# Kernel tuning notes

Hardware: AMD Instinct MI355X
Metric: run time of the kernel (lower is better)

The kernel has to match this reference:

```python
import jax, jax.numpy as jnp
import numpy as np

N_NODES = 50000
N_EDGES = 600000
F_IN = 128
HID = 128
N_GRAPHS = 512
N_CLASSES = 2


def _sage_conv(x, src, dst, Wl, Wr, b, n_nodes):
    # PyG SAGEConv (aggr='mean'): out = lin_l(mean_{j in N(i)} x_j) + lin_r(x_i)
    msg_sum = jax.ops.segment_sum(x[src], dst, num_segments=n_nodes)  # [N, F]
    deg = jax.ops.segment_sum(jnp.ones((src.shape[0],), x.dtype), dst, num_segments=n_nodes)
    agg = msg_sum / jnp.maximum(deg, 1.0)[:, None]
    return agg @ Wl + b + x @ Wr


def setup_inputs() -> dict:
    key = jax.random.key(0)
    ks = jax.random.split(key, 16)
    x = jax.random.normal(ks[0], (N_NODES, F_IN), dtype=jnp.float32)
    edge_index = jax.random.randint(ks[1], (2, N_EDGES), 0, N_NODES, dtype=jnp.int64)
    batch = jnp.sort(jax.random.randint(ks[2], (N_NODES,), 0, N_GRAPHS, dtype=jnp.int64))
    inp = {"x": x, "edge_index": edge_index, "batch": batch, "num_graphs": N_GRAPHS}
    # SAGEConv params (glorot-ish scale)
    dims = [(F_IN, HID), (HID, HID), (HID, HID), (HID, HID)]
    for i, (din, dout) in enumerate(dims, start=1):
        s = 1.0 / np.sqrt(din)
        inp[f"Wl{i}"] = jax.random.normal(ks[2 + 3 * i], (din, dout), dtype=jnp.float32) * s
        inp[f"Wr{i}"] = jax.random.normal(ks[3 + 3 * i], (din, dout), dtype=jnp.float32) * s
        inp[f"b{i}"] = jnp.zeros((dout,), dtype=jnp.float32)
    inp["Wf1"] = jax.random.normal(ks[3], (HID, 128), dtype=jnp.float32) / np.sqrt(HID)
    inp["bf1"] = jnp.zeros((128,), dtype=jnp.float32)
    inp["Wf2"] = jax.random.normal(ks[4], (128, N_CLASSES), dtype=jnp.float32) / np.sqrt(128.0)
    inp["bf2"] = jnp.zeros((N_CLASSES,), dtype=jnp.float32)
    return inp


def reference(x, edge_index, batch, num_graphs,
              Wl1, Wr1, b1, Wl2, Wr2, b2, Wl3, Wr3, b3, Wl4, Wr4, b4,
              Wf1, bf1, Wf2, bf2):
    src, dst = edge_index[0], edge_index[1]
    n = x.shape[0]
    h = jax.nn.relu(_sage_conv(x, src, dst, Wl1, Wr1, b1, n))
    h = jax.nn.relu(_sage_conv(h, src, dst, Wl2, Wr2, b2, n))
    h = jax.nn.relu(_sage_conv(h, src, dst, Wl3, Wr3, b3, n))
    h = jax.nn.relu(_sage_conv(h, src, dst, Wl4, Wr4, b4, n))
    # global_mean_pool over graphs
    pooled_sum = jax.ops.segment_sum(h, batch, num_segments=num_graphs)
    counts = jax.ops.segment_sum(jnp.ones((n,), h.dtype), batch, num_segments=num_graphs)
    pooled = pooled_sum / jnp.maximum(counts, 1.0)[:, None]
    emb = pooled @ Wf1 + bf1
    # dropout p=0.5 is identity in eval mode
    out = emb @ Wf2 + bf2
    return out
```

## Files before the change

### kernel.cpp

```cpp
#include <hip/hip_runtime.h>

#define N_NODES   50000
#define N_EDGES   600000
#define F         128
#define N_GRAPHS  512
#define MROWS     32
#define ASTRIDE   264
#define ALSTRIDE  136
#define NB_SCAN   196
#define EB        8

typedef short          short8   __attribute__((ext_vector_type(8)));
typedef float          f32x4    __attribute__((ext_vector_type(4)));
typedef unsigned int   uint4_t  __attribute__((ext_vector_type(4)));

__device__ __forceinline__ void split_bf16(float v, short& hi, short& lo) {
    unsigned u  = __float_as_uint(v);
    unsigned hb = u & 0xFFFF0000u;
    hi = (short)(u >> 16);
    float rem = v - __uint_as_float(hb);
    lo = (short)(__float_as_uint(rem) >> 16);
}

__device__ __forceinline__ unsigned short f2bf_rne(float f) {
    unsigned u = __float_as_uint(f);
    u += 0x7FFFu + ((u >> 16) & 1u);
    return (unsigned short)(u >> 16);
}

__global__ __launch_bounds__(256) void prepA_kernel(
    const float* __restrict__ x, unsigned short* __restrict__ xb,
    unsigned short* __restrict__ hb0, unsigned short* __restrict__ hb1,
    const float* __restrict__ Wl0, const float* __restrict__ Wr0,
    const float* __restrict__ Wl1, const float* __restrict__ Wr1,
    const float* __restrict__ Wl2, const float* __restrict__ Wr2,
    const float* __restrict__ Wl3, const float* __restrict__ Wr3,
    short* __restrict__ wtbase,
    const int* __restrict__ dst, int* __restrict__ deg)
{
    const int gid  = blockIdx.x * 256 + threadIdx.x;
    const int nthr = gridDim.x * 256;

    if (gid < 48) {
        int bsel = gid >> 4, c = gid & 15;
        unsigned short* p = (bsel == 0 ? xb : bsel == 1 ? hb0 : hb1)
                            + (size_t)N_NODES * F + c * 8;
        short8 z = {0,0,0,0,0,0,0,0};
        *(short8*)p = z;
    }

    for (int i = gid; i < (N_NODES * F) / 8; i += nthr) {
        float4 a = ((const float4*)x)[2 * i];
        float4 b = ((const float4*)x)[2 * i + 1];
        short8 o;
        o[0] = (short)f2bf_rne(a.x); o[1] = (short)f2bf_rne(a.y);
        o[2] = (short)f2bf_rne(a.z); o[3] = (short)f2bf_rne(a.w);
        o[4] = (short)f2bf_rne(b.x); o[5] = (short)f2bf_rne(b.y);
        o[6] = (short)f2bf_rne(b.z); o[7] = (short)f2bf_rne(b.w);
        ((short8*)xb)[i] = o;
    }

    for (int gt = gid; gt < 131072; gt += nthr) {
        int l = gt >> 15;
        int t = gt & 32767;
        const float* Wl; const float* Wr;
        switch (l) {
            case 0:  Wl = Wl0; Wr = Wr0; break;
            case 1:  Wl = Wl1; Wr = Wr1; break;
            case 2:  Wl = Wl2; Wr = Wr2; break;
            default: Wl = Wl3; Wr = Wr3; break;
        }
        int n = t >> 8, k = t & 255;
        float w = (k < F) ? Wl[k * F + n] : Wr[(k - F) * F + n];
        short h, lo;
        split_bf16(w, h, lo);
        short* hi_plane = wtbase + (size_t)l * 65536;
        hi_plane[t]         = h;
        hi_plane[32768 + t] = lo;
    }

    for (int e = gid; e < N_EDGES; e += nthr) atomicAdd(&deg[dst[e]], 1);
}

__global__ __launch_bounds__(256) void bsum_kernel(const int* __restrict__ deg,
                                                   int* __restrict__ bsum) {
    int i = blockIdx.x * 256 + threadIdx.x;
    int v = (i < N_NODES) ? deg[i] : 0;
    #pragma unroll
    for (int off = 32; off > 0; off >>= 1) v += __shfl_down(v, off, 64);
    __shared__ int wsum[4];
    if ((threadIdx.x & 63) == 0) wsum[threadIdx.x >> 6] = v;
    __syncthreads();
    if (threadIdx.x == 0) bsum[blockIdx.x] = wsum[0] + wsum[1] + wsum[2] + wsum[3];
}

__global__ __launch_bounds__(256) void scan_apply_kernel(
    const int* __restrict__ deg, const int* __restrict__ bsum,
    int* __restrict__ row_start, int* __restrict__ cursor,
    float* __restrict__ inv_deg)
{
    __shared__ int s[256];
    const int b = blockIdx.x, t = threadIdx.x;

    int v = (t < NB_SCAN) ? bsum[t] : 0;
    s[t] = v;
    __syncthreads();
    for (int off = 1; off < 256; off <<= 1) {
        int xv  = s[t];
        int add = (t >= off) ? s[t - off] : 0;
        __syncthreads();
        s[t] = xv + add;
        __syncthreads();
    }
    const int boff = (b == 0) ? 0 : s[b - 1];
    __syncthreads();

    int i = b * 256 + t;
    int d = (i < N_NODES) ? deg[i] : 0;
    s[t] = d;
    __syncthreads();
    for (int off = 1; off < 256; off <<= 1) {
        int xv  = s[t];
        int add = (t >= off) ? s[t - off] : 0;
        __syncthreads();
        s[t] = xv + add;
        __syncthreads();
    }
    int excl = s[t] - d + boff;
    if (i < N_NODES) {
        row_start[i] = excl;
        cursor[i]    = excl;
        inv_deg[i]   = 1.0f / fmaxf((float)d, 1.0f);
    }
    if (b == 0 && t == 0) row_start[N_NODES] = N_EDGES;
}

__global__ void fill_kernel(const int* __restrict__ src, const int* __restrict__ dst,
                            int* __restrict__ cursor, int* __restrict__ eidx) {
    int e = blockIdx.x * blockDim.x + threadIdx.x;
    if (e < N_EDGES) {
        int p = atomicAdd(&cursor[dst[e]], 1);
        eidx[p] = src[e];
    }
}

__global__ __launch_bounds__(512) void layer_kernel(
    const unsigned short* __restrict__ hb_in, const int* __restrict__ row_start,
    const int* __restrict__ eidx, const float* __restrict__ inv_deg,
    const short* __restrict__ wt_hi, const short* __restrict__ wt_lo,
    const float* __restrict__ b, unsigned short* __restrict__ hb_out)
{
    __shared__ short Ahi[MROWS][ASTRIDE];
    __shared__ short Alo[MROWS][ALSTRIDE];

    const int t    = threadIdx.x;
    const int base = blockIdx.x * MROWS;

    {
        const int c8  = t & 15;
        const int rr  = t >> 4;
        const int row = base + rr;
        const bool v  = (row < N_NODES);

        int a0 = 0, na = 0;
        float sc = 0.0f;
        if (v) {
            a0 = row_start[row];
            na = row_start[row + 1] - a0;
            sc = inv_deg[row];
        }

        short8 selfv = {0,0,0,0,0,0,0,0};
        if (v) selfv = *(const short8*)(hb_in + (size_t)row * F + c8 * 8);

        float acc[8] = {0,0,0,0,0,0,0,0};
        for (int eo = 0; eo < na; eo += EB) {
            int idx[EB];
            #pragma unroll
            for (int u = 0; u < EB; ++u) {
                bool ok = (eo + u) < na;
                int  sl = ok ? a0 + eo + u : a0;
                int  ia = eidx[sl];
                idx[u] = ok ? ia : N_NODES;
            }
            #pragma unroll
            for (int u = 0; u < EB; ++u) {
                short8 hv = *(const short8*)(hb_in + (size_t)idx[u] * F + c8 * 8);
                uint4_t uw = *(const uint4_t*)&hv;
                #pragma unroll
                for (int q = 0; q < 4; ++q) {
                    unsigned wq = uw[q];
                    acc[2 * q]     += __uint_as_float(wq << 16);
                    acc[2 * q + 1] += __uint_as_float(wq & 0xFFFF0000u);
                }
            }
        }

        short8 h8, l8;
        #pragma unroll
        for (int k = 0; k < 8; ++k) {
            short h, l;
            split_bf16(acc[k] * sc, h, l);
            h8[k] = h; l8[k] = l;
        }
        *(short8*)&Ahi[rr][c8 * 8] = h8;
        *(short8*)&Alo[rr][c8 * 8] = l8;
        *(short8*)&Ahi[rr][F + c8 * 8] = selfv;
    }
    __syncthreads();

    const int w    = t >> 6;
    const int lane = t & 63;
    const int m    = lane & 15;
    const int quad = lane >> 4;
    const int n0   = w * 16 + m;

    f32x4 acc0 = {0,0,0,0};
    f32x4 acc1 = {0,0,0,0};

    #pragma unroll
    for (int ks = 0; ks < 4; ++ks) {
        const int ko = ks * 32 + quad * 8;
        short8 ah0 = *(const short8*)&Ahi[m][ko];
        short8 ah1 = *(const short8*)&Ahi[16 + m][ko];
        short8 al0 = *(const short8*)&Alo[m][ko];
        short8 al1 = *(const short8*)&Alo[16 + m][ko];
        short8 bh  = *(const short8*)&wt_hi[(size_t)n0 * 256 + ko];
        short8 bl  = *(const short8*)&wt_lo[(size_t)n0 * 256 + ko];

        acc0 = __builtin_amdgcn_mfma_f32_16x16x32_bf16(ah0, bh, acc0, 0, 0, 0);
        acc0 = __builtin_amdgcn_mfma_f32_16x16x32_bf16(ah0, bl, acc0, 0, 0, 0);
        acc0 = __builtin_amdgcn_mfma_f32_16x16x32_bf16(al0, bh, acc0, 0, 0, 0);

        acc1 = __builtin_amdgcn_mfma_f32_16x16x32_bf16(ah1, bh, acc1, 0, 0, 0);
        acc1 = __builtin_amdgcn_mfma_f32_16x16x32_bf16(ah1, bl, acc1, 0, 0, 0);
        acc1 = __builtin_amdgcn_mfma_f32_16x16x32_bf16(al1, bh, acc1, 0, 0, 0);
    }
    #pragma unroll
    for (int ks = 4; ks < 8; ++ks) {
        const int ko = ks * 32 + quad * 8;
        short8 ah0 = *(const short8*)&Ahi[m][ko];
        short8 ah1 = *(const short8*)&Ahi[16 + m][ko];
        short8 bh  = *(const short8*)&wt_hi[(size_t)n0 * 256 + ko];
        short8 bl  = *(const short8*)&wt_lo[(size_t)n0 * 256 + ko];

        acc0 = __builtin_amdgcn_mfma_f32_16x16x32_bf16(ah0, bh, acc0, 0, 0, 0);
        acc0 = __builtin_amdgcn_mfma_f32_16x16x32_bf16(ah0, bl, acc0, 0, 0, 0);

        acc1 = __builtin_amdgcn_mfma_f32_16x16x32_bf16(ah1, bh, acc1, 0, 0, 0);
        acc1 = __builtin_amdgcn_mfma_f32_16x16x32_bf16(ah1, bl, acc1, 0, 0, 0);
    }

    float bj = b[n0];
    #pragma unroll
    for (int reg = 0; reg < 4; ++reg) {
        int r0 = base + quad * 4 + reg;
        int r1 = r0 + 16;
        if (r0 < N_NODES)
            hb_out[(size_t)r0 * F + n0] = f2bf_rne(fmaxf(acc0[reg] + bj, 0.0f));
        if (r1 < N_NODES)
            hb_out[(size_t)r1 * F + n0] = f2bf_rne(fmaxf(acc1[reg] + bj, 0.0f));
    }
}

__global__ __launch_bounds__(512) void poolhead_kernel(
    const int* __restrict__ batch, const unsigned short* __restrict__ hb,
    const float* __restrict__ Wf1, const float* __restrict__ bf1,
    const float* __restrict__ Wf2, const float* __restrict__ bf2,
    float* __restrict__ out)
{
    const int g   = blockIdx.x;
    const int j   = threadIdx.x & 127;
    const int grp = threadIdx.x >> 7;

    int lo = 0, hi = N_NODES;
    while (lo < hi) { int m = (lo + hi) >> 1; if (batch[m] < g) lo = m + 1; else hi = m; }
    int start = lo;
    hi = N_NODES;
    while (lo < hi) { int m = (lo + hi) >> 1; if (batch[m] <= g) lo = m + 1; else hi = m; }
    int end = lo;

    float acc = 0.0f;
    for (int r = start + grp; r < end; r += 4)
        acc += __uint_as_float((unsigned)hb[(size_t)r * F + j] << 16);

    __shared__ float part[4][F];
    __shared__ float p[F];
    __shared__ float emb[F];
    part[grp][j] = acc;
    __syncthreads();
    if (grp == 0) {
        float tot = (part[0][j] + part[1][j]) + (part[2][j] + part[3][j]);
        p[j] = tot / fmaxf((float)(end - start), 1.0f);
    }
    __syncthreads();

    float e = 0.0f;
    #pragma unroll 8
    for (int k = grp * 32; k < grp * 32 + 32; ++k) e += p[k] * Wf1[k * F + j];
    part[grp][j] = e;
    __syncthreads();
    if (grp == 0)
        emb[j] = (part[0][j] + part[1][j]) + (part[2][j] + part[3][j]) + bf1[j];
    __syncthreads();

    if (threadIdx.x < 2) {
        float o = bf2[threadIdx.x];
        for (int k = 0; k < F; ++k) o += emb[k] * Wf2[k * 2 + threadIdx.x];
        out[(size_t)g * 2 + threadIdx.x] = o;
    }
}

extern "C" void kernel_launch(void* const* d_in, const int* in_sizes, int n_in,
                              void* d_out, int out_size, void* d_ws, size_t ws_size,
                              hipStream_t stream) {
    const float* x     = (const float*)d_in[0];
    const int*   ei    = (const int*)d_in[1];
    const int*   src   = ei;
    const int*   dst   = ei + N_EDGES;
    const int*   batch = (const int*)d_in[2];
    const float* Wl0 = (const float*)d_in[4];
    const float* Wr0 = (const float*)d_in[5];
    const float* Wl1 = (const float*)d_in[7];
    const float* Wr1 = (const float*)d_in[8];
    const float* Wl2 = (const float*)d_in[10];
    const float* Wr2 = (const float*)d_in[11];
    const float* Wl3 = (const float*)d_in[13];
    const float* Wr3 = (const float*)d_in[14];
    const float* bb[4] = {(const float*)d_in[6],  (const float*)d_in[9],
                          (const float*)d_in[12], (const float*)d_in[15]};
    const float* Wf1 = (const float*)d_in[16];
    const float* bf1 = (const float*)d_in[17];
    const float* Wf2 = (const float*)d_in[18];
    const float* bf2 = (const float*)d_in[19];
    float* out = (float*)d_out;

    const size_t HSZ = (size_t)(N_NODES + 1) * F;
    unsigned short* XB  = (unsigned short*)d_ws;
    unsigned short* HB0 = XB + HSZ;
    unsigned short* HB1 = HB0 + HSZ;
    float* inv_deg   = (float*)(HB1 + HSZ);
    int*   row_start = (int*)(inv_deg + N_NODES);
    int*   cursor    = row_start + N_NODES + 1;
    int*   eidx      = cursor + N_NODES;
    int*   deg_i     = eidx + N_EDGES;
    int*   bsum      = deg_i + N_NODES;
    short* wtbase    = (short*)(bsum + 256);

    (void)hipMemsetAsync(deg_i, 0, N_NODES * sizeof(int), stream);

    prepA_kernel<<<1024, 256, 0, stream>>>(
        x, XB, HB0, HB1, Wl0, Wr0, Wl1, Wr1, Wl2, Wr2, Wl3, Wr3,
        wtbase, dst, deg_i);
    bsum_kernel<<<NB_SCAN, 256, 0, stream>>>(deg_i, bsum);
    scan_apply_kernel<<<NB_SCAN, 256, 0, stream>>>(deg_i, bsum, row_start, cursor, inv_deg);
    fill_kernel<<<(N_EDGES + 255) / 256, 256, 0, stream>>>(src, dst, cursor, eidx);

    const int layer_blocks = (N_NODES + MROWS - 1) / MROWS;
    const unsigned short* hin = XB;
    unsigned short* buf[2] = {HB0, HB1};
    for (int l = 0; l < 4; ++l) {
        unsigned short* tgt = buf[l & 1];
        const short* whi = wtbase + (size_t)l * 65536;
        const short* wlo = whi + 32768;
        layer_kernel<<<layer_blocks, 512, 0, stream>>>(
            hin, row_start, eidx, inv_deg, whi, wlo, bb[l], tgt);
        hin = tgt;
    }

    poolhead_kernel<<<N_GRAPHS, 512, 0, stream>>>(batch, hin, Wf1, bf1, Wf2, bf2, out);
}
```

Baseline: 401.4 us.

## Record edge slot during degree count and merge scan kernels

The degree-counting atomic now also returns each edge's position within its destination bucket and stores it. The CSR fill can then write directly to row_start+pos without a second atomic pass or a cursor array. The two-kernel block-sum plus scan is merged into one kernel in which each block redundantly sums all earlier counts to get its offset. This removes one launch and one round of contended atomics, at the cost of an extra 600k-int pos array and quadratic redundant reads in the scan.

Result: no change. 406.2 us, median of 2 (+1.2%).

```diff
diff --git a/kernel.cpp b/kernel.cpp
--- a/kernel.cpp
+++ b/kernel.cpp
@@ -36,7 +36,7 @@
     const float* __restrict__ Wl2, const float* __restrict__ Wr2,
     const float* __restrict__ Wl3, const float* __restrict__ Wr3,
     short* __restrict__ wtbase,
-    const int* __restrict__ dst, int* __restrict__ deg)
+    const int* __restrict__ dst, int* __restrict__ cnt, int* __restrict__ pos)
 {
     const int gid  = blockIdx.x * 256 + threadIdx.x;
     const int nthr = gridDim.x * 256;
@@ -79,31 +79,30 @@
         hi_plane[32768 + t] = lo;
     }
 
-    for (int e = gid; e < N_EDGES; e += nthr) atomicAdd(&deg[dst[e]], 1);
-}
-
-__global__ __launch_bounds__(256) void bsum_kernel(const int* __restrict__ deg,
-                                                   int* __restrict__ bsum) {
-    int i = blockIdx.x * 256 + threadIdx.x;
-    int v = (i < N_NODES) ? deg[i] : 0;
-    #pragma unroll
-    for (int off = 32; off > 0; off >>= 1) v += __shfl_down(v, off, 64);
-    __shared__ int wsum[4];
-    if ((threadIdx.x & 63) == 0) wsum[threadIdx.x >> 6] = v;
-    __syncthreads();
-    if (threadIdx.x == 0) bsum[blockIdx.x] = wsum[0] + wsum[1] + wsum[2] + wsum[3];
-}
-
-__global__ __launch_bounds__(256) void scan_apply_kernel(
-    const int* __restrict__ deg, const int* __restrict__ bsum,
-    int* __restrict__ row_start, int* __restrict__ cursor,
-    float* __restrict__ inv_deg)
+    for (int e = gid; e < N_EDGES; e += nthr)
+        pos[e] = atomicAdd(&cnt[dst[e]], 1);
+}
+
+__global__ __launch_bounds__(256) void scan2_kernel(
+    const int* __restrict__ cnt,
+    int* __restrict__ row_start, float* __restrict__ inv_deg)
 {
     __shared__ int s[256];
+    __shared__ int red[4];
     const int b = blockIdx.x, t = threadIdx.x;
 
-    int v = (t < NB_SCAN) ? bsum[t] : 0;
-    s[t] = v;
+    int partial = 0;
+    const int lim = b * 256;
+    for (int i = t; i < lim; i += 256) partial += cnt[i];
+    #pragma unroll
+    for (int off = 32; off > 0; off >>= 1) partial += __shfl_down(partial, off, 64);
+    if ((t & 63) == 0) red[t >> 6] = partial;
+    __syncthreads();
+    const int boff = red[0] + red[1] + red[2] + red[3];
+
+    int i = lim + t;
+    int d = (i < N_NODES) ? cnt[i] : 0;
+    s[t] = d;
     __syncthreads();
     for (int off = 1; off < 256; off <<= 1) {
         int xv  = s[t];
@@ -112,36 +111,20 @@
         s[t] = xv + add;
         __syncthreads();
     }
-    const int boff = (b == 0) ? 0 : s[b - 1];
-    __syncthreads();
-
-    int i = b * 256 + t;
-    int d = (i < N_NODES) ? deg[i] : 0;
-    s[t] = d;
-    __syncthreads();
-    for (int off = 1; off < 256; off <<= 1) {
-        int xv  = s[t];
-        int add = (t >= off) ? s[t - off] : 0;
-        __syncthreads();
-        s[t] = xv + add;
-        __syncthreads();
-    }
     int excl = s[t] - d + boff;
     if (i < N_NODES) {
         row_start[i] = excl;
-        cursor[i]    = excl;
         inv_deg[i]   = 1.0f / fmaxf((float)d, 1.0f);
     }
     if (b == 0 && t == 0) row_start[N_NODES] = N_EDGES;
 }
 
-__global__ void fill_kernel(const int* __restrict__ src, const int* __restrict__ dst,
-                            int* __restrict__ cursor, int* __restrict__ eidx) {
+__global__ void fill2_kernel(const int* __restrict__ src, const int* __restrict__ dst,
+                             const int* __restrict__ row_start,
+                             const int* __restrict__ pos, int* __restrict__ eidx) {
     int e = blockIdx.x * blockDim.x + threadIdx.x;
-    if (e < N_EDGES) {
-        int p = atomicAdd(&cursor[dst[e]], 1);
-        eidx[p] = src[e];
-    }
+    if (e < N_EDGES)
+        eidx[row_start[dst[e]] + pos[e]] = src[e];
 }
 
 __global__ __launch_bounds__(512) void layer_kernel(
@@ -341,20 +324,18 @@
     unsigned short* HB1 = HB0 + HSZ;
     float* inv_deg   = (float*)(HB1 + HSZ);
     int*   row_start = (int*)(inv_deg + N_NODES);
-    int*   cursor    = row_start + N_NODES + 1;
-    int*   eidx      = cursor + N_NODES;
-    int*   deg_i     = eidx + N_EDGES;
-    int*   bsum      = deg_i + N_NODES;
-    short* wtbase    = (short*)(bsum + 256);
-
-    (void)hipMemsetAsync(deg_i, 0, N_NODES * sizeof(int), stream);
+    int*   pos       = row_start + N_NODES + 1;
+    int*   eidx      = pos + N_EDGES;
+    int*   cnt       = eidx + N_EDGES;
+    short* wtbase    = (short*)(cnt + N_NODES);
+
+    (void)hipMemsetAsync(cnt, 0, N_NODES * sizeof(int), stream);
 
     prepA_kernel<<<1024, 256, 0, stream>>>(
         x, XB, HB0, HB1, Wl0, Wr0, Wl1, Wr1, Wl2, Wr2, Wl3, Wr3,
-        wtbase, dst, deg_i);
-    bsum_kernel<<<NB_SCAN, 256, 0, stream>>>(deg_i, bsum);
-    scan_apply_kernel<<<NB_SCAN, 256, 0, stream>>>(deg_i, bsum, row_start, cursor, inv_deg);
-    fill_kernel<<<(N_EDGES + 255) / 256, 256, 0, stream>>>(src, dst, cursor, eidx);
+        wtbase, dst, cnt, pos);
+    scan2_kernel<<<NB_SCAN, 256, 0, stream>>>(cnt, row_start, inv_deg);
+    fill2_kernel<<<(N_EDGES + 255) / 256, 256, 0, stream>>>(src, dst, row_start, pos, eidx);
 
     const int layer_blocks = (N_NODES + MROWS - 1) / MROWS;
     const unsigned short* hin = XB;
```
